# Kernel optimization log

Hardware: AMD Instinct MI355X
Metric: run time of the kernel (lower is better)

## Reference

```python
import jax, jax.numpy as jnp
import numpy as np

NUM_HEADS = 16
LN_EPS = 1e-5


def setup_inputs() -> dict:
    key = jax.random.key(0)
    ks = jax.random.split(key, 7)
    B, S, D = 4, 1024, 1024
    s_in = 1.0 / np.sqrt(D)
    return {
        "x": jax.random.normal(ks[0], (B, S, D), dtype=jnp.float32),
        # PyTorch MHA packed in-projection: [3D, D] weight, [3D] bias
        "w_qkv": jax.random.uniform(ks[1], (3 * D, D), dtype=jnp.float32, minval=-s_in, maxval=s_in),
        "b_qkv": jnp.zeros((3 * D,), dtype=jnp.float32),
        "w_out": jax.random.uniform(ks[2], (D, D), dtype=jnp.float32, minval=-s_in, maxval=s_in),
        "b_out": jnp.zeros((D,), dtype=jnp.float32),
        "ln_w": jnp.ones((D,), dtype=jnp.float32),
        "ln_b": jnp.zeros((D,), dtype=jnp.float32),
    }


def _layernorm(x, w, b):
    m = jnp.mean(x, axis=-1, keepdims=True)
    v = jnp.var(x, axis=-1, keepdims=True)
    return (x - m) * jax.lax.rsqrt(v + LN_EPS) * w + b


def reference(x, w_qkv, b_qkv, w_out, b_out, ln_w, ln_b):
    B, S, D = x.shape
    H = NUM_HEADS
    hd = D // H
    # packed QKV projection (torch: F.linear(x, w_qkv, b_qkv) then chunk)
    qkv = x @ w_qkv.T + b_qkv                      # [B, S, 3D]
    q, k, v = jnp.split(qkv, 3, axis=-1)
    q = q.reshape(B, S, H, hd).transpose(0, 2, 1, 3) * (hd ** -0.5)  # [B,H,S,hd]
    k = k.reshape(B, S, H, hd).transpose(0, 2, 1, 3)
    v = v.reshape(B, S, H, hd).transpose(0, 2, 1, 3)
    scores = jnp.einsum('bhqd,bhkd->bhqk', q, k)   # [B,H,S,S]
    attn = jax.nn.softmax(scores, axis=-1)
    ctx = jnp.einsum('bhqk,bhkd->bhqd', attn, v)   # [B,H,S,hd]
    ctx = ctx.transpose(0, 2, 1, 3).reshape(B, S, D)
    attn_out = ctx @ w_out.T + b_out
    # torch returns head-averaged weights (average_attn_weights=True)
    attn_weights = attn.mean(axis=1)               # [B,S,S]
    # dropout rate 0.0 -> identity; residual + LayerNorm
    y = _layernorm(x + attn_out, ln_w, ln_b)
    return y, attn_weights
```

## Files before the change

### kernel.cpp

```cpp
#include <hip/hip_runtime.h>
#include <cstdint>

typedef __bf16 bf16;
typedef __bf16 bf16x8 __attribute__((ext_vector_type(8)));
typedef __bf16 bf16x4 __attribute__((ext_vector_type(4)));
typedef float  f32x4  __attribute__((ext_vector_type(4)));

#define MFMA_BF16(a, b, c) __builtin_amdgcn_mfma_f32_16x16x32_bf16(a, b, c, 0, 0, 0)

__device__ __forceinline__ void async_load16(const void* g, void* l) {
    __builtin_amdgcn_global_load_lds(
        (__attribute__((address_space(1))) uint32_t*)(uintptr_t)g,
        (__attribute__((address_space(3))) uint32_t*)(uint32_t)(uintptr_t)l,
        16, 0, 0);
}

__global__ void cvt_kernel(const float* __restrict__ src, bf16* __restrict__ dst, int n4) {
    int i = blockIdx.x * blockDim.x + threadIdx.x;
    if (i < n4) {
        float4 v = ((const float4*)src)[i];
        bf16x4 o;
        o[0] = (bf16)v.x; o[1] = (bf16)v.y; o[2] = (bf16)v.z; o[3] = (bf16)v.w;
        ((bf16x4*)dst)[i] = o;
    }
}

__global__ __launch_bounds__(256) void gemm_qkv_kernel(
    const bf16* __restrict__ A, const bf16* __restrict__ W,
    const float* __restrict__ bias,
    bf16* __restrict__ Qb, bf16* __restrict__ Kb, bf16* __restrict__ Vt)
{
    const int Kd = 1024;
    __shared__ bf16 sA[128 * 32];
    __shared__ bf16 sB[128 * 32];
    int tid = threadIdx.x, lane = tid & 63, wid = tid >> 6;
    int m0 = blockIdx.y * 128, n0 = blockIdx.x * 128;
    int srow = wid * 32 + (lane >> 2);
    int scol = (lane & 3) * 8;
    const bf16* Ag = A + (size_t)(m0 + srow) * Kd + scol;
    const bf16* Wg = W + (size_t)(n0 + srow) * Kd + scol;
    bf16* sAp = &sA[srow * 32 + scol];
    bf16* sBp = &sB[srow * 32 + scol];
    int wm = (wid & 1) * 64, wn = (wid >> 1) * 64;
    int lcol = lane & 15, quad = lane >> 4;
    f32x4 acc[4][4] = {};
    for (int k0 = 0; k0 < Kd; k0 += 32) {
        __syncthreads();
        async_load16(Ag + k0, sAp);
        async_load16(Ag + k0 + 16 * Kd, sAp + 16 * 32);
        async_load16(Wg + k0, sBp);
        async_load16(Wg + k0 + 16 * Kd, sBp + 16 * 32);
        __syncthreads();
        bf16x8 af[4], bfr[4];
#pragma unroll
        for (int i = 0; i < 4; i++)
            af[i] = *(const bf16x8*)&sA[(wm + i * 16 + lcol) * 32 + quad * 8];
#pragma unroll
        for (int i = 0; i < 4; i++)
            bfr[i] = *(const bf16x8*)&sB[(wn + i * 16 + lcol) * 32 + quad * 8];
#pragma unroll
        for (int i = 0; i < 4; i++)
#pragma unroll
            for (int j = 0; j < 4; j++)
                acc[i][j] = MFMA_BF16(af[i], bfr[j], acc[i][j]);
    }
#pragma unroll
    for (int j = 0; j < 4; j++) {
        int n = n0 + wn + j * 16 + lcol;
        float bv = bias[n];
        int part = n >> 10, d = n & 1023, h = d >> 6, dd = d & 63;
#pragma unroll
        for (int i = 0; i < 4; i++) {
            int mb = m0 + wm + i * 16 + quad * 4;
            int b = mb >> 10, s = mb & 1023;
            if (part == 2) {
                bf16x4 v4;
#pragma unroll
                for (int r = 0; r < 4; r++) v4[r] = (bf16)(acc[i][j][r] + bv);
                *(bf16x4*)&Vt[(size_t)((b * 16 + h) * 64 + dd) * 1024 + s] = v4;
            } else {
                float scv = (part == 0) ? 0.125f : 1.0f;
                bf16* dst = (part == 0 ? Qb : Kb) + (size_t)((b * 16 + h) * 1024 + s) * 64 + dd;
#pragma unroll
                for (int r = 0; r < 4; r++) dst[(size_t)r * 64] = (bf16)((acc[i][j][r] + bv) * scv);
            }
        }
    }
}

__global__ __launch_bounds__(256) void gemm_out_kernel(
    const bf16* __restrict__ A, const bf16* __restrict__ W,
    const float* __restrict__ bias, float* __restrict__ out)
{
    const int Kd = 1024;
    __shared__ bf16 sA[128 * 32];
    __shared__ bf16 sB[128 * 32];
    int tid = threadIdx.x, lane = tid & 63, wid = tid >> 6;
    int m0 = blockIdx.y * 128, n0 = blockIdx.x * 128;
    int srow = wid * 32 + (lane >> 2);
    int scol = (lane & 3) * 8;
    const bf16* Ag = A + (size_t)(m0 + srow) * Kd + scol;
    const bf16* Wg = W + (size_t)(n0 + srow) * Kd + scol;
    bf16* sAp = &sA[srow * 32 + scol];
    bf16* sBp = &sB[srow * 32 + scol];
    int wm = (wid & 1) * 64, wn = (wid >> 1) * 64;
    int lcol = lane & 15, quad = lane >> 4;
    f32x4 acc[4][4] = {};
    for (int k0 = 0; k0 < Kd; k0 += 32) {
        __syncthreads();
        async_load16(Ag + k0, sAp);
        async_load16(Ag + k0 + 16 * Kd, sAp + 16 * 32);
        async_load16(Wg + k0, sBp);
        async_load16(Wg + k0 + 16 * Kd, sBp + 16 * 32);
        __syncthreads();
        bf16x8 af[4], bfr[4];
#pragma unroll
        for (int i = 0; i < 4; i++)
            af[i] = *(const bf16x8*)&sA[(wm + i * 16 + lcol) * 32 + quad * 8];
#pragma unroll
        for (int i = 0; i < 4; i++)
            bfr[i] = *(const bf16x8*)&sB[(wn + i * 16 + lcol) * 32 + quad * 8];
#pragma unroll
        for (int i = 0; i < 4; i++)
#pragma unroll
            for (int j = 0; j < 4; j++)
                acc[i][j] = MFMA_BF16(af[i], bfr[j], acc[i][j]);
    }
#pragma unroll
    for (int j = 0; j < 4; j++) {
        int n = n0 + wn + j * 16 + lcol;
        float bv = bias[n];
#pragma unroll
        for (int i = 0; i < 4; i++) {
            int m = m0 + wm + i * 16 + quad * 4;
#pragma unroll
            for (int r = 0; r < 4; r++) out[(size_t)(m + r) * 1024 + n] = acc[i][j][r] + bv;
        }
    }
}

#define PTS 72
__global__ __launch_bounds__(256) void flash_kernel(
    const bf16* __restrict__ Qb, const bf16* __restrict__ Kb, const bf16* __restrict__ Vt,
    bf16* __restrict__ ctx, float* __restrict__ ml)
{
    __shared__ bf16 sK[64 * 64];
    __shared__ bf16 sV[64 * 64];
    __shared__ bf16 pt[4 * 16 * PTS];
    int tid = threadIdx.x, lane = tid & 63, wid = tid >> 6;
    int bx = blockIdx.x;
    int qt = bx & 15;
    int h = (bx >> 4) & 15;
    int b = bx >> 8;
    int lcol = lane & 15, quad = lane >> 4;
    size_t base = (size_t)(b * 16 + h) * 65536;

    int q0 = qt * 64 + wid * 16;
    const bf16* qp = Qb + base + (size_t)(q0 + lcol) * 64 + quad * 8;
    bf16x8 a0 = *(const bf16x8*)qp;
    bf16x8 a1 = *(const bf16x8*)(qp + 32);

    bf16* wp = pt + wid * 16 * PTS;
    int rr8 = lane >> 3;
    int pp  = lane & 7;
    int jj  = pp ^ rr8;
    int sr0 = wid * 16 + rr8;
    int sw  = lcol & 7;

    float l_[4] = {0.f, 0.f, 0.f, 0.f};
    f32x4 o[4] = {};

    for (int kt = 0; kt < 16; kt++) {
        __syncthreads();
        async_load16(Kb + base + (size_t)(kt * 64 + sr0) * 64 + jj * 8,       &sK[sr0 * 64 + pp * 8]);
        async_load16(Kb + base + (size_t)(kt * 64 + sr0 + 8) * 64 + jj * 8,   &sK[(sr0 + 8) * 64 + pp * 8]);
        async_load16(Vt + base + (size_t)sr0 * 1024 + kt * 64 + jj * 8,       &sV[sr0 * 64 + pp * 8]);
        async_load16(Vt + base + (size_t)(sr0 + 8) * 1024 + kt * 64 + jj * 8, &sV[(sr0 + 8) * 64 + pp * 8]);
        __syncthreads();
#pragma unroll
        for (int nt = 0; nt < 4; nt++) {
            int ck = quad ^ sw;
            bf16x8 bk0 = *(const bf16x8*)&sK[(nt * 16 + lcol) * 64 + ck * 8];
            bf16x8 bk1 = *(const bf16x8*)&sK[(nt * 16 + lcol) * 64 + (ck ^ 4) * 8];
            f32x4 s = {};
            s = MFMA_BF16(a0, bk0, s);
            s = MFMA_BF16(a1, bk1, s);
#pragma unroll
            for (int rr = 0; rr < 4; rr++) {
                float p = __expf(s[rr]);
                l_[rr] += p;
                wp[(quad * 4 + rr) * PTS + nt * 16 + lcol] = (bf16)p;
            }
        }
#pragma unroll
        for (int kf = 0; kf < 2; kf++) {
            bf16x8 pa = *(const bf16x8*)&wp[lcol * PTS + kf * 32 + quad * 8];
#pragma unroll
            for (int dt = 0; dt < 4; dt++) {
                bf16x8 vb = *(const bf16x8*)&sV[(dt * 16 + lcol) * 64 + ((kf * 4 + quad) ^ sw) * 8];
                o[dt] = MFMA_BF16(pa, vb, o[dt]);
            }
        }
    }
#pragma unroll
    for (int mk = 1; mk < 16; mk <<= 1)
#pragma unroll
        for (int rr = 0; rr < 4; rr++) l_[rr] += __shfl_xor(l_[rr], mk, 64);
#pragma unroll
    for (int rr = 0; rr < 4; rr++) {
        float inv = 1.f / l_[rr];
        int qg = q0 + quad * 4 + rr;
#pragma unroll
        for (int dt = 0; dt < 4; dt++)
            ctx[(size_t)(b * 1024 + qg) * 1024 + h * 64 + dt * 16 + lcol] = (bf16)(o[dt][rr] * inv);
        if (lcol == 0)
            ml[(size_t)(b * 16 + h) * 1024 + qg] = l_[rr];
    }
}

__global__ __launch_bounds__(256) void aw_kernel(
    const bf16* __restrict__ Qb, const bf16* __restrict__ Kb,
    const float* __restrict__ ml, float* __restrict__ aw)
{
    __shared__ bf16 sK[64 * 64];
    int tid = threadIdx.x, lane = tid & 63, wid = tid >> 6;
    int bx = blockIdx.x;
    int kt = bx & 15;
    int qt = (bx >> 4) & 15;
    int b = bx >> 8;
    int lcol = lane & 15, quad = lane >> 4;
    int q0 = qt * 64 + wid * 16;
    int kbase = kt * 64;
    int sw = lcol & 7;
    float acc[16];
#pragma unroll
    for (int i = 0; i < 16; i++) acc[i] = 0.f;

    for (int h = 0; h < 16; h++) {
        size_t base = (size_t)(b * 16 + h) * 65536;
        __syncthreads();
#pragma unroll
        for (int i = 0; i < 2; i++) {
            int ci = tid + 256 * i;
            int r_ = ci >> 3;
            int pp = ci & 7;
            int jj = pp ^ (r_ & 7);
            async_load16(Kb + base + (size_t)(kbase + r_) * 64 + jj * 8, &sK[(size_t)ci * 8]);
        }
        const bf16* qp = Qb + base + (size_t)(q0 + lcol) * 64 + quad * 8;
        bf16x8 a0 = *(const bf16x8*)qp;
        bf16x8 a1 = *(const bf16x8*)(qp + 32);
        float scale[4];
#pragma unroll
        for (int rr = 0; rr < 4; rr++)
            scale[rr] = 0.0625f / ml[(size_t)(b * 16 + h) * 1024 + q0 + quad * 4 + rr];
        __syncthreads();
#pragma unroll
        for (int nt = 0; nt < 4; nt++) {
            int ck = quad ^ sw;
            bf16x8 bk0 = *(const bf16x8*)&sK[(nt * 16 + lcol) * 64 + ck * 8];
            bf16x8 bk1 = *(const bf16x8*)&sK[(nt * 16 + lcol) * 64 + (ck ^ 4) * 8];
            f32x4 s = {};
            s = MFMA_BF16(a0, bk0, s);
            s = MFMA_BF16(a1, bk1, s);
#pragma unroll
            for (int rr = 0; rr < 4; rr++)
                acc[nt * 4 + rr] += __expf(s[rr]) * scale[rr];
        }
    }
#pragma unroll
    for (int nt = 0; nt < 4; nt++)
#pragma unroll
        for (int rr = 0; rr < 4; rr++)
            aw[(size_t)(b * 1024 + q0 + quad * 4 + rr) * 1024 + kbase + nt * 16 + lcol] = acc[nt * 4 + rr];
}

__global__ __launch_bounds__(256) void ln_kernel(
    const float* __restrict__ x, const float* __restrict__ ao,
    const float* __restrict__ w, const float* __restrict__ bsh,
    float* __restrict__ y)
{
    int row = blockIdx.x, tid = threadIdx.x;
    float4 xv = ((const float4*)(x + (size_t)row * 1024))[tid];
    float4 av = ((const float4*)(ao + (size_t)row * 1024))[tid];
    float4 v = {xv.x + av.x, xv.y + av.y, xv.z + av.z, xv.w + av.w};
    float s = v.x + v.y + v.z + v.w;
    float ss = v.x * v.x + v.y * v.y + v.z * v.z + v.w * v.w;
#pragma unroll
    for (int off = 32; off; off >>= 1) { s += __shfl_down(s, off); ss += __shfl_down(ss, off); }
    __shared__ float rs[4], rss[4];
    int lane = tid & 63, wid = tid >> 6;
    if (lane == 0) { rs[wid] = s; rss[wid] = ss; }
    __syncthreads();
    s = rs[0] + rs[1] + rs[2] + rs[3];
    ss = rss[0] + rss[1] + rss[2] + rss[3];
    float mean = s * (1.f / 1024.f);
    float var = ss * (1.f / 1024.f) - mean * mean;
    float inv = rsqrtf(var + 1e-5f);
    float4 wv = ((const float4*)w)[tid];
    float4 bv = ((const float4*)bsh)[tid];
    float4 o;
    o.x = (v.x - mean) * inv * wv.x + bv.x;
    o.y = (v.y - mean) * inv * wv.y + bv.y;
    o.z = (v.z - mean) * inv * wv.z + bv.z;
    o.w = (v.w - mean) * inv * wv.w + bv.w;
    ((float4*)y)[row * 256 + tid] = o;
}

extern "C" void kernel_launch(void* const* d_in, const int* in_sizes, int n_in,
                              void* d_out, int out_size, void* d_ws, size_t ws_size,
                              hipStream_t stream) {
    const float* x     = (const float*)d_in[0];
    const float* w_qkv = (const float*)d_in[1];
    const float* b_qkv = (const float*)d_in[2];
    const float* w_out = (const float*)d_in[3];
    const float* b_out = (const float*)d_in[4];
    const float* ln_w  = (const float*)d_in[5];
    const float* ln_b  = (const float*)d_in[6];

    char* ws = (char*)d_ws;
    bf16*   Qb    = (bf16*)(ws);
    bf16*   Kb    = (bf16*)(ws + (8ull  << 20));
    bf16*   Vt    = (bf16*)(ws + (16ull << 20));
    bf16*   ctx   = (bf16*)(ws + (24ull << 20));
    float*  ml    = (float*)(ws + (32ull << 20));
    bf16*   x_bf  = (bf16*)(ws + (33ull << 20));
    bf16*   wq_bf = (bf16*)(ws + (41ull << 20));
    bf16*   wo_bf = (bf16*)(ws + (16ull << 20));
    float*  ao    = (float*)(ws);

    float* y_out  = (float*)d_out;
    float* aw_out = y_out + 4ull * 1024 * 1024;

    cvt_kernel<<<4096, 256, 0, stream>>>(x, x_bf, 1048576);
    cvt_kernel<<<3072, 256, 0, stream>>>(w_qkv, wq_bf, 786432);
    gemm_qkv_kernel<<<dim3(24, 32), 256, 0, stream>>>(x_bf, wq_bf, b_qkv, Qb, Kb, Vt);
    flash_kernel<<<1024, 256, 0, stream>>>(Qb, Kb, Vt, ctx, ml);
    aw_kernel<<<1024, 256, 0, stream>>>(Qb, Kb, ml, aw_out);
    cvt_kernel<<<1024, 256, 0, stream>>>(w_out, wo_bf, 262144);
    gemm_out_kernel<<<dim3(8, 32), 256, 0, stream>>>(ctx, wo_bf, b_out, ao);
    ln_kernel<<<4096, 256, 0, stream>>>(x, ao, ln_w, ln_b, y_out);
}
```

Baseline: 225.1 us.

## Process two 16-row query tiles per wave in flash and attention-weight kernels

Each wave now handles 32 query rows instead of 16 in both the flash attention kernel and the head-averaged attention-weight kernel, so each block covers 128 queries and the grid is halved to 512 blocks. K/V tiles loaded into shared memory are reused across twice as many queries, which halves global K/V traffic and the number of synchronisation rounds per unit of work. The cost is more registers per thread and fewer blocks (512 on a large GPU), which may reduce occupancy and latency hiding.

```diff
diff --git a/kernel.cpp b/kernel.cpp
--- a/kernel.cpp
+++ b/kernel.cpp
@@ -146,29 +146,32 @@
 {
     __shared__ bf16 sK[64 * 64];
     __shared__ bf16 sV[64 * 64];
-    __shared__ bf16 pt[4 * 16 * PTS];
+    __shared__ bf16 pt[8 * 16 * PTS];
     int tid = threadIdx.x, lane = tid & 63, wid = tid >> 6;
     int bx = blockIdx.x;
-    int qt = bx & 15;
-    int h = (bx >> 4) & 15;
-    int b = bx >> 8;
+    int qt = bx & 7;
+    int h = (bx >> 3) & 15;
+    int b = bx >> 7;
     int lcol = lane & 15, quad = lane >> 4;
     size_t base = (size_t)(b * 16 + h) * 65536;
 
-    int q0 = qt * 64 + wid * 16;
+    int q0 = qt * 128 + wid * 32;
     const bf16* qp = Qb + base + (size_t)(q0 + lcol) * 64 + quad * 8;
     bf16x8 a0 = *(const bf16x8*)qp;
     bf16x8 a1 = *(const bf16x8*)(qp + 32);
-
-    bf16* wp = pt + wid * 16 * PTS;
+    bf16x8 a2 = *(const bf16x8*)(qp + 16 * 64);
+    bf16x8 a3 = *(const bf16x8*)(qp + 16 * 64 + 32);
+
+    bf16* wpa = pt + (wid * 2) * 16 * PTS;
+    bf16* wpb = wpa + 16 * PTS;
     int rr8 = lane >> 3;
     int pp  = lane & 7;
     int jj  = pp ^ rr8;
     int sr0 = wid * 16 + rr8;
     int sw  = lcol & 7;
 
-    float l_[4] = {0.f, 0.f, 0.f, 0.f};
-    f32x4 o[4] = {};
+    float la[4] = {0.f, 0.f, 0.f, 0.f}, lb[4] = {0.f, 0.f, 0.f, 0.f};
+    f32x4 oa[4] = {}, ob[4] = {};
 
     for (int kt = 0; kt < 16; kt++) {
         __syncthreads();
@@ -182,39 +185,53 @@
             int ck = quad ^ sw;
             bf16x8 bk0 = *(const bf16x8*)&sK[(nt * 16 + lcol) * 64 + ck * 8];
             bf16x8 bk1 = *(const bf16x8*)&sK[(nt * 16 + lcol) * 64 + (ck ^ 4) * 8];
-            f32x4 s = {};
-            s = MFMA_BF16(a0, bk0, s);
-            s = MFMA_BF16(a1, bk1, s);
+            f32x4 s1 = {}, s2 = {};
+            s1 = MFMA_BF16(a0, bk0, s1); s1 = MFMA_BF16(a1, bk1, s1);
+            s2 = MFMA_BF16(a2, bk0, s2); s2 = MFMA_BF16(a3, bk1, s2);
 #pragma unroll
             for (int rr = 0; rr < 4; rr++) {
-                float p = __expf(s[rr]);
-                l_[rr] += p;
-                wp[(quad * 4 + rr) * PTS + nt * 16 + lcol] = (bf16)p;
+                float p1 = __expf(s1[rr]);
+                float p2 = __expf(s2[rr]);
+                la[rr] += p1;
+                lb[rr] += p2;
+                wpa[(quad * 4 + rr) * PTS + nt * 16 + lcol] = (bf16)p1;
+                wpb[(quad * 4 + rr) * PTS + nt * 16 + lcol] = (bf16)p2;
             }
         }
 #pragma unroll
         for (int kf = 0; kf < 2; kf++) {
-            bf16x8 pa = *(const bf16x8*)&wp[lcol * PTS + kf * 32 + quad * 8];
+            bf16x8 pa = *(const bf16x8*)&wpa[lcol * PTS + kf * 32 + quad * 8];
+            bf16x8 pb = *(const bf16x8*)&wpb[lcol * PTS + kf * 32 + quad * 8];
 #pragma unroll
             for (int dt = 0; dt < 4; dt++) {
                 bf16x8 vb = *(const bf16x8*)&sV[(dt * 16 + lcol) * 64 + ((kf * 4 + quad) ^ sw) * 8];
-                o[dt] = MFMA_BF16(pa, vb, o[dt]);
+                oa[dt] = MFMA_BF16(pa, vb, oa[dt]);
+                ob[dt] = MFMA_BF16(pb, vb, ob[dt]);
             }
         }
     }
 #pragma unroll
     for (int mk = 1; mk < 16; mk <<= 1)
 #pragma unroll
-        for (int rr = 0; rr < 4; rr++) l_[rr] += __shfl_xor(l_[rr], mk, 64);
+        for (int rr = 0; rr < 4; rr++) {
+            la[rr] += __shfl_xor(la[rr], mk, 64);
+            lb[rr] += __shfl_xor(lb[rr], mk, 64);
+        }
 #pragma unroll
     for (int rr = 0; rr < 4; rr++) {
-        float inv = 1.f / l_[rr];
-        int qg = q0 + quad * 4 + rr;
-#pragma unroll
-        for (int dt = 0; dt < 4; dt++)
-            ctx[(size_t)(b * 1024 + qg) * 1024 + h * 64 + dt * 16 + lcol] = (bf16)(o[dt][rr] * inv);
-        if (lcol == 0)
-            ml[(size_t)(b * 16 + h) * 1024 + qg] = l_[rr];
+        float inva = 1.f / la[rr];
+        float invb = 1.f / lb[rr];
+        int qa = q0 + quad * 4 + rr;
+        int qb2 = qa + 16;
+#pragma unroll
+        for (int dt = 0; dt < 4; dt++) {
+            ctx[(size_t)(b * 1024 + qa) * 1024 + h * 64 + dt * 16 + lcol]  = (bf16)(oa[dt][rr] * inva);
+            ctx[(size_t)(b * 1024 + qb2) * 1024 + h * 64 + dt * 16 + lcol] = (bf16)(ob[dt][rr] * invb);
+        }
+        if (lcol == 0) {
+            ml[(size_t)(b * 16 + h) * 1024 + qa]  = la[rr];
+            ml[(size_t)(b * 16 + h) * 1024 + qb2] = lb[rr];
+        }
     }
 }
 
@@ -226,15 +243,15 @@
     int tid = threadIdx.x, lane = tid & 63, wid = tid >> 6;
     int bx = blockIdx.x;
     int kt = bx & 15;
-    int qt = (bx >> 4) & 15;
-    int b = bx >> 8;
+    int qt = (bx >> 4) & 7;
+    int b = bx >> 7;
     int lcol = lane & 15, quad = lane >> 4;
-    int q0 = qt * 64 + wid * 16;
+    int q0 = qt * 128 + wid * 32;
     int kbase = kt * 64;
     int sw = lcol & 7;
-    float acc[16];
-#pragma unroll
-    for (int i = 0; i < 16; i++) acc[i] = 0.f;
+    float acca[16], accb[16];
+#pragma unroll
+    for (int i = 0; i < 16; i++) { acca[i] = 0.f; accb[i] = 0.f; }
 
     for (int h = 0; h < 16; h++) {
         size_t base = (size_t)(b * 16 + h) * 65536;
@@ -250,29 +267,37 @@
         const bf16* qp = Qb + base + (size_t)(q0 + lcol) * 64 + quad * 8;
         bf16x8 a0 = *(const bf16x8*)qp;
         bf16x8 a1 = *(const bf16x8*)(qp + 32);
-        float scale[4];
-#pragma unroll
-        for (int rr = 0; rr < 4; rr++)
-            scale[rr] = 0.0625f / ml[(size_t)(b * 16 + h) * 1024 + q0 + quad * 4 + rr];
+        bf16x8 a2 = *(const bf16x8*)(qp + 16 * 64);
+        bf16x8 a3 = *(const bf16x8*)(qp + 16 * 64 + 32);
+        float sca[4], scb[4];
+#pragma unroll
+        for (int rr = 0; rr < 4; rr++) {
+            sca[rr] = 0.0625f / ml[(size_t)(b * 16 + h) * 1024 + q0 + quad * 4 + rr];
+            scb[rr] = 0.0625f / ml[(size_t)(b * 16 + h) * 1024 + q0 + 16 + quad * 4 + rr];
+        }
         __syncthreads();
 #pragma unroll
         for (int nt = 0; nt < 4; nt++) {
             int ck = quad ^ sw;
             bf16x8 bk0 = *(const bf16x8*)&sK[(nt * 16 + lcol) * 64 + ck * 8];
             bf16x8 bk1 = *(const bf16x8*)&sK[(nt * 16 + lcol) * 64 + (ck ^ 4) * 8];
-            f32x4 s = {};
-            s = MFMA_BF16(a0, bk0, s);
-            s = MFMA_BF16(a1, bk1, s);
-#pragma unroll
-            for (int rr = 0; rr < 4; rr++)
-                acc[nt * 4 + rr] += __expf(s[rr]) * scale[rr];
+            f32x4 s1 = {}, s2 = {};
+            s1 = MFMA_BF16(a0, bk0, s1); s1 = MFMA_BF16(a1, bk1, s1);
+            s2 = MFMA_BF16(a2, bk0, s2); s2 = MFMA_BF16(a3, bk1, s2);
+#pragma unroll
+            for (int rr = 0; rr < 4; rr++) {
+                acca[nt * 4 + rr] += __expf(s1[rr]) * sca[rr];
+                accb[nt * 4 + rr] += __expf(s2[rr]) * scb[rr];
+            }
         }
     }
 #pragma unroll
     for (int nt = 0; nt < 4; nt++)
 #pragma unroll
-        for (int rr = 0; rr < 4; rr++)
-            aw[(size_t)(b * 1024 + q0 + quad * 4 + rr) * 1024 + kbase + nt * 16 + lcol] = acc[nt * 4 + rr];
+        for (int rr = 0; rr < 4; rr++) {
+            aw[(size_t)(b * 1024 + q0 + quad * 4 + rr) * 1024 + kbase + nt * 16 + lcol]      = acca[nt * 4 + rr];
+            aw[(size_t)(b * 1024 + q0 + 16 + quad * 4 + rr) * 1024 + kbase + nt * 16 + lcol] = accb[nt * 4 + rr];
+        }
 }
 
 __global__ __launch_bounds__(256) void ln_kernel(
@@ -335,8 +360,8 @@
     cvt_kernel<<<4096, 256, 0, stream>>>(x, x_bf, 1048576);
     cvt_kernel<<<3072, 256, 0, stream>>>(w_qkv, wq_bf, 786432);
     gemm_qkv_kernel<<<dim3(24, 32), 256, 0, stream>>>(x_bf, wq_bf, b_qkv, Qb, Kb, Vt);
-    flash_kernel<<<1024, 256, 0, stream>>>(Qb, Kb, Vt, ctx, ml);
-    aw_kernel<<<1024, 256, 0, stream>>>(Qb, Kb, ml, aw_out);
+    flash_kernel<<<512, 256, 0, stream>>>(Qb, Kb, Vt, ctx, ml);
+    aw_kernel<<<512, 256, 0, stream>>>(Qb, Kb, ml, aw_out);
     cvt_kernel<<<1024, 256, 0, stream>>>(w_out, wo_bf, 262144);
     gemm_out_kernel<<<dim3(8, 32), 256, 0, stream>>>(ctx, wo_bf, b_out, ao);
     ln_kernel<<<4096, 256, 0, stream>>>(x, ao, ln_w, ln_b, y_out);
```

After: 226.8 us. No clear change (+0.7%).
